# Kernel tuning notes

Measured on AMD Instinct MI355X. Metric: run time of the kernel, lower is better.

The kernel has to match this reference:

```python
import jax, jax.numpy as jnp
import numpy as np

NUM_CLASSES = 80
LAMBDA_COORD = 5.0
LAMBDA_NOOBJ = 0.5
FEAT_SIZES = [(80, 80), (40, 40), (20, 20)]
B, N_BOX = 32, 50


def _bce_logits(x, t):
    # BCEWithLogits, elementwise: softplus(x) - x*t (stable via logaddexp)
    return jnp.logaddexp(0.0, x) - x * t


def setup_inputs() -> dict:
    key = jax.random.key(0)
    k3, k4, k5 = jax.random.split(key, 3)
    pred_p3 = jax.random.normal(k3, (B, NUM_CLASSES + 5, 80, 80), dtype=jnp.float32)
    pred_p4 = jax.random.normal(k4, (B, NUM_CLASSES + 5, 40, 40), dtype=jnp.float32)
    pred_p5 = jax.random.normal(k5, (B, NUM_CLASSES + 5, 20, 20), dtype=jnp.float32)
    # Targets: 50 boxes/image with distinct cells at the coarsest (20x20) scale
    # (=> distinct at every scale), so scatter assignment is unambiguous.
    rng = np.random.default_rng(0)
    cells = np.stack([rng.choice(400, N_BOX, replace=False) for _ in range(B)])  # [B,N]
    cy, cx = cells // 20, cells % 20
    u = rng.random((B, N_BOX, 2))
    x = (cx + u[..., 0]) / 20.0
    y = (cy + u[..., 1]) / 20.0
    w = rng.uniform(0.05, 0.3, (B, N_BOX))
    h = rng.uniform(0.05, 0.3, (B, N_BOX))
    tgt_boxes = jnp.asarray(np.stack([x, y, w, h], axis=-1).astype(np.float32))  # [B,N,4]
    tgt_cls = jnp.asarray(rng.integers(0, NUM_CLASSES, (B, N_BOX)).astype(np.int32))
    return {"pred_p3": pred_p3, "pred_p4": pred_p4, "pred_p5": pred_p5,
            "tgt_boxes": tgt_boxes, "tgt_cls": tgt_cls}


def _scale_losses(pred, feat_h, feat_w, tgt_boxes, tgt_cls):
    # pred: [B, C+5, H, W] -> [B, H, W, C+5]
    p = jnp.transpose(pred, (0, 2, 3, 1))
    pb, po, pc = p[..., :4], p[..., 4], p[..., 5:]
    bsz, nbox = tgt_boxes.shape[0], tgt_boxes.shape[1]
    gx = jnp.clip((tgt_boxes[..., 0] * feat_w).astype(jnp.int32), 0, feat_w - 1)
    gy = jnp.clip((tgt_boxes[..., 1] * feat_h).astype(jnp.int32), 0, feat_h - 1)
    bi = jnp.broadcast_to(jnp.arange(bsz)[:, None], (bsz, nbox))
    obj = jnp.zeros((bsz, feat_h, feat_w), jnp.float32).at[bi, gy, gx].set(1.0)
    tbox = jnp.zeros((bsz, feat_h, feat_w, 4), jnp.float32).at[bi, gy, gx].set(tgt_boxes)
    tcls = jnp.zeros((bsz, feat_h, feat_w, NUM_CLASSES), jnp.float32).at[bi, gy, gx].set(
        jax.nn.one_hot(tgt_cls, NUM_CLASSES, dtype=jnp.float32))
    bce_obj = _bce_logits(po, obj)                                  # [B,H,W]
    obj_loss = jnp.mean(bce_obj, axis=(1, 2)) + LAMBDA_NOOBJ * jnp.mean(bce_obj * (1.0 - obj), axis=(1, 2))
    bbox_loss = LAMBDA_COORD * jnp.sum(obj[..., None] * (pb - tbox) ** 2, axis=(1, 2, 3))
    n_obj = jnp.sum(obj, axis=(1, 2))
    cls_sum = jnp.sum(obj[..., None] * _bce_logits(pc, tcls), axis=(1, 2, 3))
    cls_loss = jnp.where(n_obj > 0, cls_sum / jnp.maximum(n_obj * NUM_CLASSES, 1.0), 0.0)
    return bbox_loss, obj_loss, cls_loss  # each [B]


def reference(pred_p3, pred_p4, pred_p5, tgt_boxes, tgt_cls):
    preds = [pred_p3, pred_p4, pred_p5]
    bbox = obj = cls = 0.0
    for pred, (fh, fw) in zip(preds, FEAT_SIZES):
        bl, ol, cl = _scale_losses(pred, fh, fw, tgt_boxes, tgt_cls)
        bbox = bbox + jnp.sum(bl)
        obj = obj + jnp.sum(ol)
        cls = cls + jnp.sum(cl)
    denom = pred_p3.shape[0] * len(preds)
    bbox, obj, cls = bbox / denom, obj / denom, cls / denom
    total = bbox + obj + cls
    return jnp.stack([bbox, obj, cls, total])
```

## Files before the change

### kernel.cpp

```cpp
#include <hip/hip_runtime.h>
#include <math.h>


#define DENSE_V4_TOTAL 67200
#define DENSE_BLOCKS 263
#define SP_GROUPS 22
#define SP_WAVES 2112
#define SPARSE_BLOCKS 528
#define TOTAL_BLOCKS (DENSE_BLOCKS + SPARSE_BLOCKS)

__device__ __forceinline__ float softplusf(float x) {
    return fmaxf(x, 0.0f) + log1pf(__expf(-fabsf(x)));
}

__global__ __launch_bounds__(256)
void yolo_loss_partial(const float* __restrict__ p3,
                       const float* __restrict__ p4,
                       const float* __restrict__ p5,
                       const float* __restrict__ tb,
                       const int*   __restrict__ tc,
                       float* __restrict__ ws)
{
    const int lane = threadIdx.x & 63;
    const int wid  = threadIdx.x >> 6;
    __shared__ float red[4][3];

    float vb = 0.f, vo = 0.f, vc = 0.f;

    if (blockIdx.x < DENSE_BLOCKS) {
        int i = blockIdx.x * 256 + threadIdx.x;
        if (i < DENSE_V4_TOTAL) {
            const float* dp; float dscale;
            if (i < 51200) {
                int b = i / 1600, o = i - b * 1600;
                dp = p3 + ((size_t)b * 85 + 4) * 6400 + o * 4;
                dscale = 1.5f / 6400.f;
            } else if (i < 64000) {
                int j = i - 51200;
                int b = j / 400, o = j - b * 400;
                dp = p4 + ((size_t)b * 85 + 4) * 1600 + o * 4;
                dscale = 1.5f / 1600.f;
            } else {
                int j = i - 64000;
                int b = j / 100, o = j - b * 100;
                dp = p5 + ((size_t)b * 85 + 4) * 400 + o * 4;
                dscale = 1.5f / 400.f;
            }
            float4 dv = *(const float4*)dp;
            vo = (softplusf(dv.x) + softplusf(dv.y) +
                  softplusf(dv.z) + softplusf(dv.w)) * dscale;
        }
    } else {
        int w  = (blockIdx.x - DENSE_BLOCKS) * 4 + wid;
        int sb = w / SP_GROUPS;
        int g  = w - sb * SP_GROUPS;
        int s  = sb >> 5;
        int b  = sb & 31;
        int c0 = g * 4;

        const float* pred; int fw, hw; float invHW;
        if (s == 0)      { pred = p3; fw = 80; hw = 6400; invHW = 1.f / 6400.f; }
        else if (s == 1) { pred = p4; fw = 40; hw = 1600; invHW = 1.f / 1600.f; }
        else             { pred = p5; fw = 20; hw = 400;  invHW = 1.f / 400.f;  }

        if (lane < 50) {
            const float4 t4 = *(const float4*)(tb + ((size_t)(b * 50 + lane)) * 4);
            int tgt = tc[b * 50 + lane];

            int gx = (int)(t4.x * (float)fw); gx = min(max(gx, 0), fw - 1);
            int gy = (int)(t4.y * (float)fw); gy = min(max(gy, 0), fw - 1);
            const float* base = pred + (size_t)b * 85 * hw + gy * fw + gx;

            float v0 = base[(size_t)c0 * hw];
            float v1 = (c0 + 1 < 85) ? base[(size_t)(c0 + 1) * hw] : 0.f;
            float v2 = (c0 + 2 < 85) ? base[(size_t)(c0 + 2) * hw] : 0.f;
            float v3 = (c0 + 3 < 85) ? base[(size_t)(c0 + 3) * hw] : 0.f;

            if (g == 0) {
                float d0 = v0 - t4.x, d1 = v1 - t4.y;
                float d2 = v2 - t4.z, d3 = v3 - t4.w;
                vb = d0 * d0 + d1 * d1 + d2 * d2 + d3 * d3;
            } else if (g == 1) {
                vo  = -(v0 + 0.5f * softplusf(v0)) * invHW;
                vc  = softplusf(v1) - (0 == tgt ? v1 : 0.f);
                vc += softplusf(v2) - (1 == tgt ? v2 : 0.f);
                vc += softplusf(v3) - (2 == tgt ? v3 : 0.f);
            } else {
                vc  = softplusf(v0) - ((c0 - 5) == tgt ? v0 : 0.f);
                if (c0 + 1 < 85) vc += softplusf(v1) - ((c0 - 4) == tgt ? v1 : 0.f);
                if (c0 + 2 < 85) vc += softplusf(v2) - ((c0 - 3) == tgt ? v2 : 0.f);
                if (c0 + 3 < 85) vc += softplusf(v3) - ((c0 - 2) == tgt ? v3 : 0.f);
            }
        }
    }

    vb *= (5.f / 96.f);
    vo *= (1.f / 96.f);
    vc *= (1.f / (4000.f * 96.f));

    #pragma unroll
    for (int off = 1; off < 64; off <<= 1) {
        vb += __shfl_xor(vb, off, 64);
        vo += __shfl_xor(vo, off, 64);
        vc += __shfl_xor(vc, off, 64);
    }

    if (lane == 0) { red[wid][0] = vb; red[wid][1] = vo; red[wid][2] = vc; }
    __syncthreads();
    if (threadIdx.x == 0) {
        float b0 = red[0][0] + red[1][0] + red[2][0] + red[3][0];
        float o0 = red[0][1] + red[1][1] + red[2][1] + red[3][1];
        float c0s = red[0][2] + red[1][2] + red[2][2] + red[3][2];
        ((float4*)ws)[blockIdx.x] = make_float4(b0, o0, c0s, 0.f);
    }
}

__global__ __launch_bounds__(256)
void yolo_loss_final(const float* __restrict__ ws, float* __restrict__ out)
{
    const int lane = threadIdx.x & 63;
    const int wid  = threadIdx.x >> 6;
    __shared__ float red[4][3];

    float sb = 0.f, so = 0.f, sc = 0.f;
    for (int i = threadIdx.x; i < TOTAL_BLOCKS; i += 256) {
        const float4 v = ((const float4*)ws)[i];
        sb += v.x; so += v.y; sc += v.z;
    }
    #pragma unroll
    for (int off = 1; off < 64; off <<= 1) {
        sb += __shfl_xor(sb, off, 64);
        so += __shfl_xor(so, off, 64);
        sc += __shfl_xor(sc, off, 64);
    }
    if (lane == 0) { red[wid][0] = sb; red[wid][1] = so; red[wid][2] = sc; }
    __syncthreads();
    if (threadIdx.x == 0) {
        float b0 = red[0][0] + red[1][0] + red[2][0] + red[3][0];
        float o0 = red[0][1] + red[1][1] + red[2][1] + red[3][1];
        float c0 = red[0][2] + red[1][2] + red[2][2] + red[3][2];
        out[0] = b0;
        out[1] = o0;
        out[2] = c0;
        out[3] = b0 + o0 + c0;
    }
}

extern "C" void kernel_launch(void* const* d_in, const int* in_sizes, int n_in,
                              void* d_out, int out_size, void* d_ws, size_t ws_size,
                              hipStream_t stream) {
    const float* p3 = (const float*)d_in[0];
    const float* p4 = (const float*)d_in[1];
    const float* p5 = (const float*)d_in[2];
    const float* tb = (const float*)d_in[3];
    const int*   tc = (const int*)d_in[4];
    float* out = (float*)d_out;
    float* ws  = (float*)d_ws;

    hipLaunchKernelGGL(yolo_loss_partial,
                       dim3(TOTAL_BLOCKS), dim3(256), 0, stream,
                       p3, p4, p5, tb, tc, ws);
    hipLaunchKernelGGL(yolo_loss_final,
                       dim3(1), dim3(256), 0, stream,
                       ws, out);
}
```

Measured before the change: 14.03 us.

## Stream full P4/P5 tensors with shared-memory box maps instead of sparse gathers

```diff
diff --git a/kernel.cpp b/kernel.cpp
--- a/kernel.cpp
+++ b/kernel.cpp
@@ -2,12 +2,14 @@
 #include <math.h>
 
 
-#define DENSE_V4_TOTAL 67200
-#define DENSE_BLOCKS 263
-#define SP_GROUPS 22
-#define SP_WAVES 2112
-#define SPARSE_BLOCKS 528
-#define TOTAL_BLOCKS (DENSE_BLOCKS + SPARSE_BLOCKS)
+#define P3D_BLOCKS 200
+#define P4_BLOCKS  256
+#define P5_BLOCKS  64
+#define P3G_BLOCKS 176
+#define NB_P3D P3D_BLOCKS
+#define NB_P4  (NB_P3D + P4_BLOCKS)
+#define NB_P5  (NB_P4 + P5_BLOCKS)
+#define TOTAL_BLOCKS (NB_P5 + P3G_BLOCKS)
 
 __device__ __forceinline__ float softplusf(float x) {
     return fmaxf(x, 0.0f) + log1pf(__expf(-fabsf(x)));
@@ -24,57 +26,91 @@
     const int lane = threadIdx.x & 63;
     const int wid  = threadIdx.x >> 6;
     __shared__ float red[4][3];
+    __shared__ signed char boxid[200];
+    __shared__ float tbox[200];
+    __shared__ int   tgs[50];
 
     float vb = 0.f, vo = 0.f, vc = 0.f;
-
-    if (blockIdx.x < DENSE_BLOCKS) {
-        int i = blockIdx.x * 256 + threadIdx.x;
-        if (i < DENSE_V4_TOTAL) {
-            const float* dp; float dscale;
-            if (i < 51200) {
-                int b = i / 1600, o = i - b * 1600;
-                dp = p3 + ((size_t)b * 85 + 4) * 6400 + o * 4;
-                dscale = 1.5f / 6400.f;
-            } else if (i < 64000) {
-                int j = i - 51200;
-                int b = j / 400, o = j - b * 400;
-                dp = p4 + ((size_t)b * 85 + 4) * 1600 + o * 4;
-                dscale = 1.5f / 1600.f;
-            } else {
-                int j = i - 64000;
-                int b = j / 100, o = j - b * 100;
-                dp = p5 + ((size_t)b * 85 + 4) * 400 + o * 4;
-                dscale = 1.5f / 400.f;
-            }
-            float4 dv = *(const float4*)dp;
+    const int blk = blockIdx.x;
+
+    if (blk < NB_P3D) {
+        int i = blk * 256 + threadIdx.x;
+        if (i < 51200) {
+            int b = i / 1600, o = i - b * 1600;
+            const float4 dv = *(const float4*)(p3 + ((size_t)b * 85 + 4) * 6400 + o * 4);
             vo = (softplusf(dv.x) + softplusf(dv.y) +
-                  softplusf(dv.z) + softplusf(dv.w)) * dscale;
-        }
-    } else {
-        int w  = (blockIdx.x - DENSE_BLOCKS) * 4 + wid;
-        int sb = w / SP_GROUPS;
-        int g  = w - sb * SP_GROUPS;
-        int s  = sb >> 5;
-        int b  = sb & 31;
-        int c0 = g * 4;
-
-        const float* pred; int fw, hw; float invHW;
-        if (s == 0)      { pred = p3; fw = 80; hw = 6400; invHW = 1.f / 6400.f; }
-        else if (s == 1) { pred = p4; fw = 40; hw = 1600; invHW = 1.f / 1600.f; }
-        else             { pred = p5; fw = 20; hw = 400;  invHW = 1.f / 400.f;  }
-
-        if (lane < 50) {
-            const float4 t4 = *(const float4*)(tb + ((size_t)(b * 50 + lane)) * 4);
-            int tgt = tc[b * 50 + lane];
-
+                  softplusf(dv.z) + softplusf(dv.w)) * (1.5f / 6400.f);
+        }
+    } else if (blk < NB_P5) {
+        const float* pred; int fw, hw, b, c0; float invHW;
+        if (blk < NB_P4) {
+            int j = blk - NB_P3D; b = j >> 3; c0 = (j & 7) * 200;
+            pred = p4; fw = 40; hw = 1600; invHW = 1.f / 1600.f;
+        } else {
+            int j = blk - NB_P4; b = j >> 1; c0 = (j & 1) * 200;
+            pred = p5; fw = 20; hw = 400; invHW = 1.f / 400.f;
+        }
+
+        for (int i = threadIdx.x; i < 200; i += 256) boxid[i] = (signed char)-1;
+        __syncthreads();
+        if (threadIdx.x < 50) {
+            const float4 t4 = *(const float4*)(tb + (size_t)(b * 50 + threadIdx.x) * 4);
+            tbox[threadIdx.x * 4 + 0] = t4.x;
+            tbox[threadIdx.x * 4 + 1] = t4.y;
+            tbox[threadIdx.x * 4 + 2] = t4.z;
+            tbox[threadIdx.x * 4 + 3] = t4.w;
+            tgs[threadIdx.x] = tc[b * 50 + threadIdx.x];
             int gx = (int)(t4.x * (float)fw); gx = min(max(gx, 0), fw - 1);
             int gy = (int)(t4.y * (float)fw); gy = min(max(gy, 0), fw - 1);
-            const float* base = pred + (size_t)b * 85 * hw + gy * fw + gx;
-
-            float v0 = base[(size_t)c0 * hw];
-            float v1 = (c0 + 1 < 85) ? base[(size_t)(c0 + 1) * hw] : 0.f;
-            float v2 = (c0 + 2 < 85) ? base[(size_t)(c0 + 2) * hw] : 0.f;
-            float v3 = (c0 + 3 < 85) ? base[(size_t)(c0 + 3) * hw] : 0.f;
+            int rel = gy * fw + gx - c0;
+            if (rel >= 0 && rel < 200) boxid[rel] = (signed char)threadIdx.x;
+        }
+        __syncthreads();
+
+        const float* bp = pred + (size_t)b * 85 * hw + c0;
+        auto proc = [&](float vv, int ch, int rel) {
+            int bid = boxid[rel];
+            if (ch == 4) {
+                float s = softplusf(vv);
+                vo += 1.5f * s * invHW;
+                if (bid >= 0) vo -= (vv + 0.5f * s) * invHW;
+            } else if (bid >= 0) {
+                if (ch < 4) {
+                    float d = vv - tbox[bid * 4 + ch];
+                    vb += d * d;
+                } else {
+                    vc += softplusf(vv) - ((ch - 5) == tgs[bid] ? vv : 0.f);
+                }
+            }
+        };
+        for (int i4 = threadIdx.x; i4 < 85 * 50; i4 += 256) {
+            int ch = i4 / 50, c4 = i4 - ch * 50;
+            const float4 v = *(const float4*)(bp + (size_t)ch * hw + c4 * 4);
+            int rel = c4 * 4;
+            proc(v.x, ch, rel + 0);
+            proc(v.y, ch, rel + 1);
+            proc(v.z, ch, rel + 2);
+            proc(v.w, ch, rel + 3);
+        }
+    } else {
+        int w = (blk - NB_P5) * 4 + wid;
+        int b = w / 22;
+        int g = w - b * 22;
+        int c0 = g * 4;
+        const float invHW = 1.f / 6400.f;
+
+        if (lane < 50) {
+            const float4 t4 = *(const float4*)(tb + (size_t)(b * 50 + lane) * 4);
+            int tgt = tc[b * 50 + lane];
+
+            int gx = (int)(t4.x * 80.f); gx = min(max(gx, 0), 79);
+            int gy = (int)(t4.y * 80.f); gy = min(max(gy, 0), 79);
+            const float* base = p3 + (size_t)b * 85 * 6400 + gy * 80 + gx;
+
+            float v0 = base[(size_t)c0 * 6400];
+            float v1 = (c0 + 1 < 85) ? base[(size_t)(c0 + 1) * 6400] : 0.f;
+            float v2 = (c0 + 2 < 85) ? base[(size_t)(c0 + 2) * 6400] : 0.f;
+            float v3 = (c0 + 3 < 85) ? base[(size_t)(c0 + 3) * 6400] : 0.f;
 
             if (g == 0) {
                 float d0 = v0 - t4.x, d1 = v1 - t4.y;
```

Result: slower. 46.11 us (+228.6%).
